# Performance work log

Measured on AMD Instinct MI355X. Metric: run time of the kernel, lower is better.

Reference implementation:

```python
import jax, jax.numpy as jnp
import numpy as np

B, RES_IN, STRIDE, RES_OUT = 8, 64, 2, 32
C_IN, C_OUT = 256, 512
H, KD, RATIO = 8, 16, 4
VD = RATIO * KD                      # 64
KV_DIM = (RATIO + 1) * KD * H        # 640
Q_DIM = KD * H                       # 128
PROJ_IN = RATIO * KD * H             # 512
SEQ = RES_IN * RES_IN                # 4096
QLEN = RES_OUT * RES_OUT             # 1024
EPS = 1e-3                           # keras BatchNormalization default epsilon


def _bn(x, gamma, beta, mean, var):
    # inference-mode batch norm over the channel axis
    return (x - mean) * (gamma * jax.lax.rsqrt(var + EPS)) + beta


def _hard_swish(x):
    return x * jnp.clip(x + 3.0, 0.0, 6.0) * (1.0 / 6.0)


def setup_inputs() -> dict:
    key = jax.random.key(0)
    ks = jax.random.split(key, 16)
    def lin(k, fan_in, fan_out):
        return jax.random.normal(k, (fan_in, fan_out), jnp.float32) / np.sqrt(fan_in)
    def bn_params(k, c):
        k1, k2, k3 = jax.random.split(k, 3)
        gamma = 1.0 + 0.1 * jax.random.normal(k1, (c,), jnp.float32)
        beta = 0.1 * jax.random.normal(k2, (c,), jnp.float32)
        mean = 0.1 * jax.random.normal(k3, (c,), jnp.float32)
        var = jax.random.uniform(jax.random.fold_in(k, 7), (c,), jnp.float32, 0.5, 1.5)
        return gamma, beta, mean, var
    x = jax.random.normal(ks[0], (B, SEQ, C_IN), jnp.float32)
    Wkv = lin(ks[1], C_IN, KV_DIM); bkv = jnp.zeros((KV_DIM,), jnp.float32)
    g_kv, b_kv, m_kv, v_kv = bn_params(ks[2], KV_DIM)
    Wq = lin(ks[3], C_IN, Q_DIM); bq = jnp.zeros((Q_DIM,), jnp.float32)
    g_q, b_q, m_q, v_q = bn_params(ks[4], Q_DIM)
    Wp = lin(ks[5], PROJ_IN, C_OUT); bp = jnp.zeros((C_OUT,), jnp.float32)
    g_p, b_p, m_p, v_p = bn_params(ks[6], C_OUT)
    return {"x": x, "Wkv": Wkv, "bkv": bkv, "g_kv": g_kv, "b_kv": b_kv, "m_kv": m_kv, "v_kv": v_kv,
            "Wq": Wq, "bq": bq, "g_q": g_q, "b_q": b_q, "m_q": m_q, "v_q": v_q,
            "Wp": Wp, "bp": bp, "g_p": g_p, "b_p": b_p, "m_p": m_p, "v_p": v_p}


def reference(x, Wkv, bkv, g_kv, b_kv, m_kv, v_kv,
              Wq, bq, g_q, b_q, m_q, v_q,
              Wp, bp, g_p, b_p, m_p, v_p):
    scale = KD ** (-0.5)
    # keys/values: Dense + BN -> [B, SEQ, H, KD+VD]
    kv = _bn(x @ Wkv + bkv, g_kv, b_kv, m_kv, v_kv)
    kv = kv.reshape(B, SEQ, H, KD + VD)
    k = jnp.transpose(kv[..., :KD], (0, 2, 1, 3))          # [B, H, SEQ, KD]
    v = jnp.transpose(kv[..., KD:], (0, 2, 1, 3))          # [B, H, SEQ, VD]
    # strided query subsample: [B, SEQ, C] -> [B, QLEN, C]
    xq = x.reshape(B, RES_IN, RES_IN, C_IN)[:, ::STRIDE, ::STRIDE].reshape(B, QLEN, C_IN)
    q = _bn(xq @ Wq + bq, g_q, b_q, m_q, v_q)
    q = jnp.transpose(q.reshape(B, QLEN, H, KD), (0, 2, 1, 3))  # [B, H, QLEN, KD]
    attn = jnp.einsum('bhqd,bhkd->bhqk', q, k) * scale
    attn = jax.nn.softmax(attn, axis=-1)                   # [B, H, QLEN, SEQ]
    av = jnp.einsum('bhqk,bhkd->bhqd', attn, v)            # [B, H, QLEN, VD]
    # faithful to TF: transpose (0,1,3,2) then reshape to (B, -1, PROJ_IN)
    out = jnp.transpose(av, (0, 1, 3, 2)).reshape(B, -1, PROJ_IN)
    out = _bn(_hard_swish(out) @ Wp + bp, g_p, b_p, m_p, v_p)
    return out
```

## Files before the change

### kernel.cpp

```cpp
#include <hip/hip_runtime.h>

typedef __bf16 bf16_t;
typedef __bf16 bf16x4 __attribute__((ext_vector_type(4)));
typedef __bf16 bf16x8 __attribute__((ext_vector_type(8)));
typedef short s16x4 __attribute__((ext_vector_type(4)));
typedef float f32x4 __attribute__((ext_vector_type(4)));

#define BN_EPS 1e-3f

#define GLOAD_LDS16(g, l) \
  __builtin_amdgcn_global_load_lds((const __attribute__((address_space(1))) void*)(g), \
                                   (__attribute__((address_space(3))) void*)(l), 16, 0, 0)

__global__ __launch_bounds__(256) void prep(
    const float* __restrict__ x, bf16_t* __restrict__ xb,
    const float* __restrict__ Wkv, bf16_t* __restrict__ outK, bf16_t* __restrict__ outV,
    const float* __restrict__ Wq, bf16_t* __restrict__ Wq_t,
    const float* __restrict__ Wp, bf16_t* __restrict__ Wp_t)
{
  __shared__ bf16_t t[32][33];
  const int id = blockIdx.x;
  if (id < 4096) {
    long i = ((long)id * 256 + threadIdx.x) * 8;
    f32x4 a = *(const f32x4*)(x + i);
    f32x4 b = *(const f32x4*)(x + i + 4);
    bf16x8 o;
    o[0] = (bf16_t)a[0]; o[1] = (bf16_t)a[1]; o[2] = (bf16_t)a[2]; o[3] = (bf16_t)a[3];
    o[4] = (bf16_t)b[0]; o[5] = (bf16_t)b[1]; o[6] = (bf16_t)b[2]; o[7] = (bf16_t)b[3];
    *(bf16x8*)(xb + i) = o;
    return;
  }
  const int tx = threadIdx.x & 31, ty = threadIdx.x >> 5;
  if (id < 4256) {
    int id2 = id - 4096;
    int bx = (id2 % 20) * 32, by = (id2 / 20) * 32;
#pragma unroll
    for (int i = 0; i < 32; i += 8)
      t[ty + i][tx] = (bf16_t)Wkv[(long)(by + ty + i) * 640 + (bx + tx)];
    __syncthreads();
#pragma unroll
    for (int i = 0; i < 32; i += 8) {
      int c = bx + ty + i;
      int h = c / 80, r80 = c - h * 80;
      bf16_t v = t[tx][ty + i];
      if (r80 < 16)
        outK[(long)(h * 16 + r80) * 256 + (by + tx)] = v;
      else
        outV[(long)(h * 64 + (r80 - 16)) * 256 + (by + tx)] = v;
    }
  } else if (id < 4288) {
    int id3 = id - 4256;
    int bx = (id3 & 3) * 32, by = (id3 >> 2) * 32;
#pragma unroll
    for (int i = 0; i < 32; i += 8)
      t[ty + i][tx] = (bf16_t)Wq[(long)(by + ty + i) * 128 + (bx + tx)];
    __syncthreads();
#pragma unroll
    for (int i = 0; i < 32; i += 8)
      Wq_t[(long)(bx + ty + i) * 256 + (by + tx)] = t[tx][ty + i];
  } else {
    int id4 = id - 4288;
    int bx = (id4 & 15) * 32, by = (id4 >> 4) * 32;
#pragma unroll
    for (int i = 0; i < 32; i += 8)
      t[ty + i][tx] = (bf16_t)Wp[(long)(by + ty + i) * 512 + (bx + tx)];
    __syncthreads();
#pragma unroll
    for (int i = 0; i < 32; i += 8)
      Wp_t[(long)(bx + ty + i) * 512 + (by + tx)] = t[tx][ty + i];
  }
}

__global__ __launch_bounds__(512, 1) void qkv_fused(
    const bf16_t* __restrict__ xb, const bf16_t* __restrict__ Wf,
    const float* __restrict__ bkv, const float* __restrict__ g_kv,
    const float* __restrict__ b_kv, const float* __restrict__ m_kv,
    const float* __restrict__ v_kv,
    const float* __restrict__ bq, const float* __restrict__ g_q,
    const float* __restrict__ b_q, const float* __restrict__ m_q,
    const float* __restrict__ v_q,
    bf16_t* __restrict__ Kbuf, bf16_t* __restrict__ Vtb, bf16_t* __restrict__ Qbuf)
{
  __shared__ __align__(16) char Xs[65536];
  __shared__ __align__(16) char Ws[65536];

  const int tid = threadIdx.x;
  const int lane = tid & 63, w = tid >> 6;
  const int quad = lane >> 4, l15 = lane & 15;
  const int wm = w >> 2, wn = w & 3;

  const int id = blockIdx.x;
  const int xcd = id & 7, slot = id >> 3;
  const int sd6 = slot / 6;
  const int mt = xcd * 32 + sd6;
  const int nt = slot - sd6 * 6;
  const int blockM = mt * 128, blockN = nt * 128;

  {
    const int r_lo = w * 2 + (lane >> 5);
    const int soff = ((lane & 31) ^ (r_lo & 7)) << 4;
#pragma unroll
    for (int rnd = 0; rnd < 8; rnd++) {
      const int row = rnd * 16 + r_lo;
      GLOAD_LDS16((const char*)xb + (long)(blockM + row) * 512 + soff,
                  &Xs[rnd * 8192 + w * 1024]);
      GLOAD_LDS16((const char*)Wf + (long)(blockN + row) * 512 + soff,
                  &Ws[rnd * 8192 + w * 1024]);
    }
  }
  __syncthreads();

  const int sw = l15 & 7;
  f32x4 acc[4][2] = {};
#pragma unroll
  for (int ks = 0; ks < 8; ks++) {
    const int u = ks * 4 + quad;
    const int su = (u ^ sw) << 4;
    bf16x8 af[4];
#pragma unroll
    for (int mi = 0; mi < 4; mi++)
      af[mi] = *(const bf16x8*)(&Xs[(wm * 64 + mi * 16 + l15) * 512 + su]);
    bf16x8 bf_[2];
#pragma unroll
    for (int ni = 0; ni < 2; ni++)
      bf_[ni] = *(const bf16x8*)(&Ws[(wn * 32 + ni * 16 + l15) * 512 + su]);
#pragma unroll
    for (int mi = 0; mi < 4; mi++)
#pragma unroll
      for (int ni = 0; ni < 2; ni++)
        acc[mi][ni] = __builtin_amdgcn_mfma_f32_16x16x32_bf16(af[mi], bf_[ni], acc[mi][ni], 0, 0, 0);
  }

#pragma unroll
  for (int ni = 0; ni < 2; ni++) {
    const int nfbase = blockN + wn * 32 + ni * 16;
    const int col = nfbase + l15;
    float s, t, bia;
    if (nfbase < 128) {
      int cp = (col >> 4) * 80 + (col & 15);
      s = g_kv[cp] / sqrtf(v_kv[cp] + BN_EPS);
      t = b_kv[cp] - m_kv[cp] * s;
      bia = bkv[cp];
      int h = col >> 4, d = col & 15;
#pragma unroll
      for (int mi = 0; mi < 4; mi++)
#pragma unroll
        for (int r = 0; r < 4; r++) {
          int grow = blockM + wm * 64 + mi * 16 + quad * 4 + r;
          int b = grow >> 12, seq = grow & 4095;
          float y = (acc[mi][ni][r] + bia) * s + t;
          Kbuf[((long)((b * 8 + h) * 4096 + seq)) * 16 + d] = (bf16_t)y;
        }
    } else if (nfbase < 640) {
      int ch = col - 128;
      int cp = (ch >> 6) * 80 + 16 + (ch & 63);
      s = g_kv[cp] / sqrtf(v_kv[cp] + BN_EPS);
      t = b_kv[cp] - m_kv[cp] * s;
      bia = bkv[cp];
      int h2 = ch >> 6, dv = ch & 63;
#pragma unroll
      for (int mi = 0; mi < 4; mi++)
#pragma unroll
        for (int r = 0; r < 4; r++) {
          int grow = blockM + wm * 64 + mi * 16 + quad * 4 + r;
          int b = grow >> 12, seq = grow & 4095;
          int kb = seq >> 5, s32 = seq & 31;
          int qd = (s32 & 15) >> 2, j = (s32 >> 4) * 4 + (s32 & 3);
          float y = (acc[mi][ni][r] + bia) * s + t;
          Vtb[(((long)(b * 8 + h2)) << 18) + (kb << 11) + (qd << 9) + (dv << 3) + j] = (bf16_t)y;
        }
    } else {
      int qc = col - 640;
      s = g_q[qc] / sqrtf(v_q[qc] + BN_EPS);
      t = b_q[qc] - m_q[qc] * s;
      bia = bq[qc];
      int h = qc >> 4, d = qc & 15;
#pragma unroll
      for (int mi = 0; mi < 4; mi++) {
        if ((((blockM + wm * 64 + mi * 16) >> 6) & 1) != 0) continue;
#pragma unroll
        for (int r = 0; r < 4; r += 2) {
          int grow = blockM + wm * 64 + mi * 16 + quad * 4 + r;
          int b = grow >> 12, seq = grow & 4095;
          int qp = ((seq >> 7) << 5) + ((seq & 63) >> 1);
          float y = (acc[mi][ni][r] + bia) * s + t;
          Qbuf[((long)((b * 8 + h) * 1024 + qp)) * 16 + d] = (bf16_t)(y * 0.36067376f);
        }
      }
    }
  }
}

__global__ __launch_bounds__(512, 1) void proj_fused(
    const bf16_t* __restrict__ A, const bf16_t* __restrict__ Wt,
    const float* __restrict__ bias, const float* __restrict__ gamma,
    const float* __restrict__ beta, const float* __restrict__ mean,
    const float* __restrict__ var, float* __restrict__ outf)
{
  __shared__ __align__(16) char Xs[65536];
  __shared__ __align__(16) char Wl[65536];

  const int tid = threadIdx.x;
  const int lane = tid & 63, w = tid >> 6;
  const int quad = lane >> 4, l15 = lane & 15;
  const int wm = w >> 2, wn = w & 3;

  const int id = blockIdx.x;
  const int xcd = id & 7, slot = id >> 3;
  const int mt = xcd * 8 + (slot >> 2);
  const int nt = slot & 3;
  const int blockM = mt * 128, blockN = nt * 128;

  const int r_lo = w * 2 + (lane >> 5);
  const int soff = ((lane & 31) ^ (r_lo & 7)) << 4;
  const int sw = l15 & 7;
  f32x4 acc[4][2] = {};

#pragma unroll
  for (int kc = 0; kc < 2; kc++) {
    if (kc) __syncthreads();
#pragma unroll
    for (int rnd = 0; rnd < 8; rnd++) {
      const int row = rnd * 16 + r_lo;
      GLOAD_LDS16((const char*)A  + (long)(blockM + row) * 1024 + kc * 512 + soff,
                  &Xs[rnd * 8192 + w * 1024]);
      GLOAD_LDS16((const char*)Wt + (long)(blockN + row) * 1024 + kc * 512 + soff,
                  &Wl[rnd * 8192 + w * 1024]);
    }
    __syncthreads();

#pragma unroll
    for (int ks = 0; ks < 8; ks++) {
      const int u = ks * 4 + quad;
      const int su = (u ^ sw) << 4;
      bf16x8 af[4];
#pragma unroll
      for (int mi = 0; mi < 4; mi++)
        af[mi] = *(const bf16x8*)(&Xs[(wm * 64 + mi * 16 + l15) * 512 + su]);
      bf16x8 bw[2];
#pragma unroll
      for (int ni = 0; ni < 2; ni++)
        bw[ni] = *(const bf16x8*)(&Wl[(wn * 32 + ni * 16 + l15) * 512 + su]);
#pragma unroll
      for (int mi = 0; mi < 4; mi++)
#pragma unroll
        for (int ni = 0; ni < 2; ni++)
          acc[mi][ni] = __builtin_amdgcn_mfma_f32_16x16x32_bf16(af[mi], bw[ni], acc[mi][ni], 0, 0, 0);
    }
  }

#pragma unroll
  for (int ni = 0; ni < 2; ni++) {
    int col = blockN + wn * 32 + ni * 16 + l15;
    float s = gamma[col] / sqrtf(var[col] + BN_EPS);
    float t = beta[col] - mean[col] * s;
    float bia = bias[col];
#pragma unroll
    for (int mi = 0; mi < 4; mi++)
#pragma unroll
      for (int r = 0; r < 4; r++) {
        int grow = blockM + wm * 64 + mi * 16 + quad * 4 + r;
        float y = (acc[mi][ni][r] + bia) * s + t;
        outf[(long)grow * 512 + col] = y;
      }
  }
}

__global__ __launch_bounds__(256, 2) void attn_kernel(
    const bf16_t* __restrict__ Q, const bf16_t* __restrict__ K,
    const bf16_t* __restrict__ Vt, bf16_t* __restrict__ outp)
{
  const int tid = threadIdx.x;
  const int lane = tid & 63, w = tid >> 6;
  const int quad = lane >> 4, l15 = lane & 15;
  const int bh = blockIdx.x & 63, qb = blockIdx.x >> 6;
  const int b = bh >> 3, h = bh & 7;
  const bf16_t* Qp = Q + (long)bh * 1024 * 16;
  const char* Kg = (const char*)(K + (long)bh * 4096 * 16);
  const char* Vg = (const char*)(Vt + ((long)bh << 18));

  __shared__ __align__(16) char Kl[4][2048];
  __shared__ __align__(16) char Vl[4][8192];

  const int q0 = qb * 128 + w * 32;
  bf16x8 qB8[2];
#pragma unroll
  for (int g = 0; g < 2; g++) {
    bf16x8 qv = *(const bf16x8*)(Qp + (long)(q0 + g * 16 + l15) * 16 + (quad & 1) * 8);
    bf16x8 zq = {};
    qB8[g] = (quad < 2) ? qv : zq;
  }

  f32x4 O[2][4] = {};
  f32x4 lpacc[2] = {};
  const f32x4 zf = {0.f, 0.f, 0.f, 0.f};

  bf16x8 ones8;
#pragma unroll
  for (int i = 0; i < 8; i++) ones8[i] = (bf16_t)1.f;

  const char* vsrc = Vg + (long)lane * 16;
  const char* ksrc = Kg + (long)lane * 32 + (w - 2) * 16;

  auto stage = [&](int t, int buf) {
    if (w < 2) {
#pragma unroll
      for (int c = 0; c < 2; c++)
        GLOAD_LDS16(vsrc + (long)t * 8192 + (w * 2 + c) * 1024, &Vl[buf][(w * 2 + c) * 1024]);
    } else {
#pragma unroll
      for (int c = 0; c < 2; c++)
        GLOAD_LDS16(vsrc + (long)t * 8192 + ((w - 2) * 2 + 4 + c) * 1024,
                    &Vl[buf][((w - 2) * 2 + 4 + c) * 1024]);
      GLOAD_LDS16(ksrc + (long)t * 2048, &Kl[buf][(w - 2) * 1024]);
    }
  };

  const int krow_off = (quad & 1) * 1024;

  auto compute = [&](int buf) {
#pragma unroll
    for (int kh = 0; kh < 2; kh++) {
      bf16x8 k0 = *(const bf16x8*)(&Kl[buf][krow_off + (kh * 32 + l15) * 16]);
      bf16x8 k1 = *(const bf16x8*)(&Kl[buf][krow_off + (kh * 32 + 16 + l15) * 16]);
      bf16x8 vA[4];
#pragma unroll
      for (int dt = 0; dt < 4; dt++)
        vA[dt] = *(const bf16x8*)(&Vl[buf][kh * 4096 + quad * 1024 + (dt * 16 + l15) * 16]);
#pragma unroll
      for (int g = 0; g < 2; g++) {
        f32x4 S0 = __builtin_amdgcn_mfma_f32_16x16x32_bf16(k0, qB8[g], zf, 0, 0, 0);
        f32x4 S1 = __builtin_amdgcn_mfma_f32_16x16x32_bf16(k1, qB8[g], zf, 0, 0, 0);
        bf16x8 pb;
        pb[0] = (bf16_t)__builtin_amdgcn_exp2f(S0[0]);
        pb[1] = (bf16_t)__builtin_amdgcn_exp2f(S0[1]);
        pb[2] = (bf16_t)__builtin_amdgcn_exp2f(S0[2]);
        pb[3] = (bf16_t)__builtin_amdgcn_exp2f(S0[3]);
        pb[4] = (bf16_t)__builtin_amdgcn_exp2f(S1[0]);
        pb[5] = (bf16_t)__builtin_amdgcn_exp2f(S1[1]);
        pb[6] = (bf16_t)__builtin_amdgcn_exp2f(S1[2]);
        pb[7] = (bf16_t)__builtin_amdgcn_exp2f(S1[3]);
        lpacc[g] = __builtin_amdgcn_mfma_f32_16x16x32_bf16(ones8, pb, lpacc[g], 0, 0, 0);
#pragma unroll
        for (int dt = 0; dt < 4; dt++)
          O[g][dt] = __builtin_amdgcn_mfma_f32_16x16x32_bf16(vA[dt], pb, O[g][dt], 0, 0, 0);
      }
    }
  };

  stage(0, 0);
  stage(1, 1);
  stage(2, 2);
#pragma unroll 4
  for (int t = 0; t < 64; t++) {
    if (t + 2 < 64) {
      if (w < 2) asm volatile("s_waitcnt vmcnt(4)" ::: "memory");
      else       asm volatile("s_waitcnt vmcnt(6)" ::: "memory");
    } else if (t + 1 < 64) {
      if (w < 2) asm volatile("s_waitcnt vmcnt(2)" ::: "memory");
      else       asm volatile("s_waitcnt vmcnt(3)" ::: "memory");
    } else {
      asm volatile("s_waitcnt vmcnt(0)" ::: "memory");
    }
    __builtin_amdgcn_s_barrier();
    __builtin_amdgcn_sched_barrier(0);
    if (t + 3 < 64) stage(t + 3, (t + 3) & 3);
    compute(t & 3);
  }

#pragma unroll
  for (int g = 0; g < 2; g++) {
    float rl = __builtin_amdgcn_rcpf(lpacc[g][0]);
    int q = q0 + g * 16 + l15;
    long colq = q & 511;
    long rowbase = (long)b * 1024 + (long)h * 128 + (q >> 9);
#pragma unroll
    for (int dt = 0; dt < 4; dt++) {
#pragma unroll
      for (int r = 0; r < 4; r++) {
        int dv = dt * 16 + quad * 4 + r;
        float val = O[g][dt][r] * rl;
        float hs = val * fminf(fmaxf(val + 3.f, 0.f), 6.f) * (1.f / 6.f);
        outp[(rowbase + (long)dv * 2) * 512 + colq] = (bf16_t)hs;
      }
    }
  }
}

extern "C" void kernel_launch(void* const* d_in, const int* in_sizes, int n_in,
                              void* d_out, int out_size, void* d_ws, size_t ws_size,
                              hipStream_t stream)
{
  const float* x    = (const float*)d_in[0];
  const float* Wkv  = (const float*)d_in[1];
  const float* bkv  = (const float*)d_in[2];
  const float* g_kv = (const float*)d_in[3];
  const float* b_kv = (const float*)d_in[4];
  const float* m_kv = (const float*)d_in[5];
  const float* v_kv = (const float*)d_in[6];
  const float* Wq   = (const float*)d_in[7];
  const float* bq   = (const float*)d_in[8];
  const float* g_q  = (const float*)d_in[9];
  const float* b_q  = (const float*)d_in[10];
  const float* m_q  = (const float*)d_in[11];
  const float* v_q  = (const float*)d_in[12];
  const float* Wp   = (const float*)d_in[13];
  const float* bp   = (const float*)d_in[14];
  const float* g_p  = (const float*)d_in[15];
  const float* b_p  = (const float*)d_in[16];
  const float* m_p  = (const float*)d_in[17];
  const float* v_p  = (const float*)d_in[18];

  char* ws = (char*)d_ws;
  bf16_t* xb   = (bf16_t*)ws; ws += (long)8 * 4096 * 256 * 2;
  bf16_t* WkT  = (bf16_t*)ws; ws += (long)128 * 256 * 2;
  bf16_t* WvT  = (bf16_t*)ws; ws += (long)512 * 256 * 2;
  bf16_t* Wq_t = (bf16_t*)ws; ws += (long)128 * 256 * 2;
  bf16_t* Wp_t = (bf16_t*)ws; ws += (long)512 * 512 * 2;
  bf16_t* Qbuf = (bf16_t*)ws; ws += (long)64 * 1024 * 16 * 2;
  bf16_t* Kbuf = (bf16_t*)ws; ws += (long)64 * 4096 * 16 * 2;
  bf16_t* Vtb  = (bf16_t*)ws; ws += (long)64 * 64 * 4096 * 2;
  bf16_t* outp = (bf16_t*)ws; ws += (long)8192 * 512 * 2;
  ws += 16384;

  prep<<<dim3(4544), 256, 0, stream>>>(x, xb, Wkv, WkT, WvT, Wq, Wq_t, Wp, Wp_t);

  qkv_fused<<<dim3(1536), 512, 0, stream>>>(xb, WkT,
      bkv, g_kv, b_kv, m_kv, v_kv, bq, g_q, b_q, m_q, v_q,
      Kbuf, Vtb, Qbuf);

  attn_kernel<<<dim3(512), 256, 0, stream>>>(Qbuf, Kbuf, Vtb, outp);

  proj_fused<<<dim3(256), 512, 0, stream>>>(outp, Wp_t, bp, g_p, b_p, m_p, v_p, (float*)d_out);
}
```

Baseline: 208.9 us.

## Split attention blocks to two waves, batch QK MFMAs and raise priority

The attention kernel now runs 1024 blocks of 128 threads, each covering 64 queries instead of 128, so the grid has twice as many blocks over the 256 CUs. The staging loads are spread evenly across the two waves, with the vmcnt waits changed to match. The compute step issues all four QK score MFMAs first, then all the exp2 calls, then the PV MFMAs under raised s_setprio, to give more instruction-level parallelism. The cost is that each K/V tile is loaded into LDS twice as often per query processed, which doubles L2 traffic for K and V.

Result: no change. 210.3 us (+0.7%).

```diff
diff --git a/kernel.cpp b/kernel.cpp
--- a/kernel.cpp
+++ b/kernel.cpp
@@ -266,7 +266,7 @@
   }
 }
 
-__global__ __launch_bounds__(256, 2) void attn_kernel(
+__global__ __launch_bounds__(128, 2) void attn_kernel(
     const bf16_t* __restrict__ Q, const bf16_t* __restrict__ K,
     const bf16_t* __restrict__ Vt, bf16_t* __restrict__ outp)
 {
@@ -282,7 +282,7 @@
   __shared__ __align__(16) char Kl[4][2048];
   __shared__ __align__(16) char Vl[4][8192];
 
-  const int q0 = qb * 128 + w * 32;
+  const int q0 = qb * 64 + w * 32;
   bf16x8 qB8[2];
 #pragma unroll
   for (int g = 0; g < 2; g++) {
@@ -299,53 +299,57 @@
 #pragma unroll
   for (int i = 0; i < 8; i++) ones8[i] = (bf16_t)1.f;
 
-  const char* vsrc = Vg + (long)lane * 16;
-  const char* ksrc = Kg + (long)lane * 32 + (w - 2) * 16;
+  const char* vsrc = Vg + (long)lane * 16 + (long)(w * 4) * 1024;
+  const char* ksrc = Kg + (long)lane * 32 + w * 16;
 
   auto stage = [&](int t, int buf) {
-    if (w < 2) {
-#pragma unroll
-      for (int c = 0; c < 2; c++)
-        GLOAD_LDS16(vsrc + (long)t * 8192 + (w * 2 + c) * 1024, &Vl[buf][(w * 2 + c) * 1024]);
-    } else {
-#pragma unroll
-      for (int c = 0; c < 2; c++)
-        GLOAD_LDS16(vsrc + (long)t * 8192 + ((w - 2) * 2 + 4 + c) * 1024,
-                    &Vl[buf][((w - 2) * 2 + 4 + c) * 1024]);
-      GLOAD_LDS16(ksrc + (long)t * 2048, &Kl[buf][(w - 2) * 1024]);
-    }
+#pragma unroll
+    for (int c = 0; c < 4; c++)
+      GLOAD_LDS16(vsrc + (long)t * 8192 + c * 1024, &Vl[buf][(w * 4 + c) * 1024]);
+    GLOAD_LDS16(ksrc + (long)t * 2048, &Kl[buf][w * 1024]);
   };
 
   const int krow_off = (quad & 1) * 1024;
 
   auto compute = [&](int buf) {
-#pragma unroll
-    for (int kh = 0; kh < 2; kh++) {
-      bf16x8 k0 = *(const bf16x8*)(&Kl[buf][krow_off + (kh * 32 + l15) * 16]);
-      bf16x8 k1 = *(const bf16x8*)(&Kl[buf][krow_off + (kh * 32 + 16 + l15) * 16]);
-      bf16x8 vA[4];
+    bf16x8 kf[4];
+#pragma unroll
+    for (int kg = 0; kg < 4; kg++)
+      kf[kg] = *(const bf16x8*)(&Kl[buf][krow_off + (kg * 16 + l15) * 16]);
+    bf16x8 vA[2][4];
+#pragma unroll
+    for (int kh = 0; kh < 2; kh++)
 #pragma unroll
       for (int dt = 0; dt < 4; dt++)
-        vA[dt] = *(const bf16x8*)(&Vl[buf][kh * 4096 + quad * 1024 + (dt * 16 + l15) * 16]);
+        vA[kh][dt] = *(const bf16x8*)(&Vl[buf][kh * 4096 + quad * 1024 + (dt * 16 + l15) * 16]);
+    f32x4 S[4][2];
+#pragma unroll
+    for (int kg = 0; kg < 4; kg++)
+#pragma unroll
+      for (int g = 0; g < 2; g++)
+        S[kg][g] = __builtin_amdgcn_mfma_f32_16x16x32_bf16(kf[kg], qB8[g], zf, 0, 0, 0);
+    bf16x8 pb[2][2];
+#pragma unroll
+    for (int kh = 0; kh < 2; kh++)
 #pragma unroll
       for (int g = 0; g < 2; g++) {
-        f32x4 S0 = __builtin_amdgcn_mfma_f32_16x16x32_bf16(k0, qB8[g], zf, 0, 0, 0);
-        f32x4 S1 = __builtin_amdgcn_mfma_f32_16x16x32_bf16(k1, qB8[g], zf, 0, 0, 0);
-        bf16x8 pb;
-        pb[0] = (bf16_t)__builtin_amdgcn_exp2f(S0[0]);
-        pb[1] = (bf16_t)__builtin_amdgcn_exp2f(S0[1]);
-        pb[2] = (bf16_t)__builtin_amdgcn_exp2f(S0[2]);
-        pb[3] = (bf16_t)__builtin_amdgcn_exp2f(S0[3]);
-        pb[4] = (bf16_t)__builtin_amdgcn_exp2f(S1[0]);
-        pb[5] = (bf16_t)__builtin_amdgcn_exp2f(S1[1]);
-        pb[6] = (bf16_t)__builtin_amdgcn_exp2f(S1[2]);
-        pb[7] = (bf16_t)__builtin_amdgcn_exp2f(S1[3]);
-        lpacc[g] = __builtin_amdgcn_mfma_f32_16x16x32_bf16(ones8, pb, lpacc[g], 0, 0, 0);
+#pragma unroll
+        for (int r = 0; r < 4; r++) {
+          pb[kh][g][r]     = (bf16_t)__builtin_amdgcn_exp2f(S[2 * kh][g][r]);
+          pb[kh][g][4 + r] = (bf16_t)__builtin_amdgcn_exp2f(S[2 * kh + 1][g][r]);
+        }
+      }
+    __builtin_amdgcn_s_setprio(1);
+#pragma unroll
+    for (int kh = 0; kh < 2; kh++)
+#pragma unroll
+      for (int g = 0; g < 2; g++) {
+        lpacc[g] = __builtin_amdgcn_mfma_f32_16x16x32_bf16(ones8, pb[kh][g], lpacc[g], 0, 0, 0);
 #pragma unroll
         for (int dt = 0; dt < 4; dt++)
-          O[g][dt] = __builtin_amdgcn_mfma_f32_16x16x32_bf16(vA[dt], pb, O[g][dt], 0, 0, 0);
+          O[g][dt] = __builtin_amdgcn_mfma_f32_16x16x32_bf16(vA[kh][dt], pb[kh][g], O[g][dt], 0, 0, 0);
       }
-    }
+    __builtin_amdgcn_s_setprio(0);
   };
 
   stage(0, 0);
@@ -353,12 +357,10 @@
   stage(2, 2);
 #pragma unroll 4
   for (int t = 0; t < 64; t++) {
-    if (t + 2 < 64) {
-      if (w < 2) asm volatile("s_waitcnt vmcnt(4)" ::: "memory");
-      else       asm volatile("s_waitcnt vmcnt(6)" ::: "memory");
-    } else if (t + 1 < 64) {
-      if (w < 2) asm volatile("s_waitcnt vmcnt(2)" ::: "memory");
-      else       asm volatile("s_waitcnt vmcnt(3)" ::: "memory");
+    if (t <= 61) {
+      asm volatile("s_waitcnt vmcnt(10)" ::: "memory");
+    } else if (t == 62) {
+      asm volatile("s_waitcnt vmcnt(5)" ::: "memory");
     } else {
       asm volatile("s_waitcnt vmcnt(0)" ::: "memory");
     }
@@ -429,7 +431,7 @@
       bkv, g_kv, b_kv, m_kv, v_kv, bq, g_q, b_q, m_q, v_q,
       Kbuf, Vtb, Qbuf);
 
-  attn_kernel<<<dim3(512), 256, 0, stream>>>(Qbuf, Kbuf, Vtb, outp);
+  attn_kernel<<<dim3(1024), 128, 0, stream>>>(Qbuf, Kbuf, Vtb, outp);
 
   proj_fused<<<dim3(256), 512, 0, stream>>>(outp, Wp_t, bp, g_p, b_p, m_p, v_p, (float*)d_out);
 }
```
